# Kernel optimization log

Measured on AMD Instinct MI355X. Metric: run time of the kernel, lower is better.

The kernel has to match this reference:

```python
import jax, jax.numpy as jnp
import numpy as np

TRAJ_NUM = 8
EVAL = 30
SGM_T = 2.0
D0 = 0.5
R = 0.3
VOX = 0.2


def setup_inputs() -> dict:
    key = jax.random.key(0)
    ks = jax.random.split(key, 6)
    G, M = 256, 4
    B = G * TRAJ_NUM
    nx, ny, nz = 400, 400, 64
    # quintic boundary matrix at t=0 and t=T; L = A^{-1}
    T = SGM_T
    A = np.array([
        [1, 0, 0, 0, 0, 0],
        [0, 1, 0, 0, 0, 0],
        [0, 0, 2, 0, 0, 0],
        [1, T, T**2, T**3, T**4, T**5],
        [0, 1, 2*T, 3*T**2, 4*T**3, 5*T**4],
        [0, 0, 2, 6*T, 12*T**2, 20*T**3]], dtype=np.float64)
    L = jnp.asarray(np.linalg.inv(A), dtype=jnp.float32)

    def state(k):
        kp, kv, ka = jax.random.split(k, 3)
        # positions inside the 80m x 80m x 12.8m map, away from borders
        p = jax.random.uniform(kp, (B, 3)) * jnp.array([70.0, 70.0, 10.0]) + jnp.array([5.0, 5.0, 1.0])
        v = jax.random.uniform(kv, (B, 3), minval=-1.0, maxval=1.0)
        a = jax.random.uniform(ka, (B, 3), minval=-0.5, maxval=0.5)
        return jnp.stack([p, v, a], axis=-1)  # (B,3,3): rows=axis, cols=[p,v,a]

    Df = state(ks[0])
    Dp = state(ks[1])
    sdf_maps = jax.random.normal(ks[2], (M, nz, ny, nx), dtype=jnp.float32) * 0.5 + 1.0  # (M,D,H,W)
    min_bounds = jnp.zeros((M, 3), jnp.float32)
    sdf_shapes = jnp.tile(jnp.array([[nx, ny, nz]], jnp.float32), (M, 1))  # (nx,ny,nz)
    map_id = jax.random.randint(ks[3], (G,), 0, M)
    return dict(Df=Df, Dp=Dp, L=L, sdf_maps=sdf_maps, min_bounds=min_bounds,
                sdf_shapes=sdf_shapes, map_id=map_id)


def _distance_cost(pos, map_id, sdf_maps, min_bounds, sdf_shapes):
    # pos: (G,N,3) world coords; replicates get_batch_sdf + grid_sample math
    mb = min_bounds[map_id]                           # (G,3)
    shp = sdf_shapes[map_id].astype(jnp.int32)        # (G,3) = (nx,ny,nz)
    mn = jnp.trunc((pos.min(1) - mb) / VOX).astype(jnp.int32)
    mx = jnp.trunc((pos.max(1) - mb) / VOX).astype(jnp.int32)
    max_spans = (mx - mn).max(0)                      # (3,) shared crop span
    c = (mn + mx) // 2
    mn = c - max_spans // 2 - 5
    mx = c + max_spans // 2 + 5
    nmn = jnp.maximum(mn, 0)
    mx = mx + (nmn - mn)
    mn = nmn
    nmx = jnp.minimum(mx, shp)
    mn = mn - (mx - nmx)
    mx = nmx
    shift = jnp.maximum(-jnp.minimum(mn, 0), 0).max(0)  # per-axis over batch
    mn = mn + shift
    local_origin = mn.astype(pos.dtype) * VOX + mb     # (G,3)
    lshape = mx - mn                                   # (G,3) int, crop size

    grid = (pos - local_origin[:, None, :]) / VOX      # local voxel coords (x,y,z)
    gp = 2.0 * grid / (lshape - 1).astype(pos.dtype)[:, None, :] - 1.0
    valid = jnp.all((gp < 0.99) & (gp > -0.99), axis=-1)  # (G,N)

    # trilinear sample, align_corners=True, zeros padding w.r.t. the crop;
    # crop voxel (i,j,k) == full-map voxel (i,j,k)+mn, so gather from the full map
    l0 = jnp.floor(grid).astype(jnp.int32)
    f = grid - l0
    Dm, Hm, Wm = sdf_maps.shape[1:]
    acc = jnp.zeros(pos.shape[:2], pos.dtype)
    for dx in (0, 1):
        for dy in (0, 1):
            for dz in (0, 1):
                il = l0 + jnp.array([dx, dy, dz], jnp.int32)       # (G,N,3) local corner
                inb = jnp.all((il >= 0) & (il < lshape[:, None, :]), axis=-1)
                ig = il + mn[:, None, :]                            # global voxel index
                gx = jnp.clip(ig[..., 0], 0, Wm - 1)
                gy = jnp.clip(ig[..., 1], 0, Hm - 1)
                gz = jnp.clip(ig[..., 2], 0, Dm - 1)
                val = sdf_maps[map_id[:, None], gz, gy, gx]         # (G,N)
                w = ((f[..., 0] if dx else 1 - f[..., 0]) *
                     (f[..., 1] if dy else 1 - f[..., 1]) *
                     (f[..., 2] if dz else 1 - f[..., 2]))
                acc = acc + jnp.where(inb, w * val, 0.0)
    dist = acc
    cost = jnp.exp(-(dist - D0) / R)
    cost = jnp.where(valid, cost, 0.0)
    return cost, dist


def reference(Df, Dp, L, sdf_maps, min_bounds, sdf_shapes, map_id):
    B = Dp.shape[0]
    # coefficients: per axis, coe = L @ [Df_row, Dp_row]
    d = jnp.concatenate([Df, Dp], axis=-1)          # (B,3,6)
    coe = jnp.einsum('jk,bik->bij', L, d)           # (B,3,6)
    dt = SGM_T / EVAL
    t = jnp.linspace(dt, SGM_T, EVAL)               # (30,)
    tp = t[:, None] ** jnp.arange(6)                # (30,6) Vandermonde
    pos = jnp.einsum('nk,bik->bni', tp, coe)        # (B,30,3)
    G = B // TRAJ_NUM
    pos_batch = pos.reshape(G, TRAJ_NUM * EVAL, 3)  # (G,N,3)
    cost, _ = _distance_cost(pos_batch, map_id, sdf_maps, min_bounds, sdf_shapes)
    cost_colli = (cost * dt).reshape(-1, EVAL).sum(-1)  # (B,)
    return cost_colli
```

## Files before the change

### kernel.cpp

```cpp
#include <hip/hip_runtime.h>
#include <hip/hip_bf16.h>
#include <math.h>

#define TRAJ 8
#define EV   30
#define NPT  (TRAJ*EV)
#define GCONST 256
#define MCONST 4
#define NXM  400
#define NYM  400
#define NZM  64

__device__ __forceinline__ float ldf(const void* p, int idx, int isbf) {
    if (isbf) return __bfloat162float(((const __hip_bfloat16*)p)[idx]);
    return ((const float*)p)[idx];
}

__device__ __forceinline__ void resolve_ms(const void*& minb,
                                           const void*& shapes) {
    if (*(const unsigned*)shapes == 0u) {
        const void* t = minb; minb = shapes; shapes = t;
    }
}

__device__ __forceinline__ int detect_bf16(const void* shapes) {
    return *(const unsigned*)shapes != 0x43C80000u;
}

__device__ __forceinline__ void build_coe(const void* Df, const void* Dp,
                                          const void* L, int g, int isbf,
                                          float* sL, float* scoe, int t) {
#pragma clang fp contract(off)
    if (t < 36) sL[t] = ldf(L, t, isbf);
    __syncthreads();
    if (t < 144) {
        int traj = t / 18, rem = t % 18, i = rem / 6, j = rem % 6;
        int b = g * TRAJ + traj;
        float dv[6];
#pragma unroll
        for (int k = 0; k < 3; ++k) {
            dv[k]     = ldf(Df, b * 9 + i * 3 + k, isbf);
            dv[3 + k] = ldf(Dp, b * 9 + i * 3 + k, isbf);
        }
        float s = 0.f;
#pragma unroll
        for (int k = 0; k < 6; ++k) s = s + sL[j * 6 + k] * dv[k];
        scoe[(traj * 3 + i) * 6 + j] = s;
    }
    __syncthreads();
}

__device__ __forceinline__ void eval_pos(const float* scoe, int traj, int e,
                                         double* p) {
    const double dt   = 2.0 / 30.0;
    const double step = (2.0 - dt) / 29.0;
    double tn = (e == EV - 1) ? 2.0 : dt + (double)e * step;
    double tk = 1.0;
    p[0] = p[1] = p[2] = 0.0;
#pragma unroll
    for (int k = 0; k < 6; ++k) {
        p[0] += tk * (double)scoe[(traj * 3 + 0) * 6 + k];
        p[1] += tk * (double)scoe[(traj * 3 + 1) * 6 + k];
        p[2] += tk * (double)scoe[(traj * 3 + 2) * 6 + k];
        tk *= tn;
    }
}

__device__ __forceinline__ void sample_and_reduce(
    const void* minb, const void* shapes, const void* sdf, int isbf, int mid,
    int g, int t, const int* mnf, const int* lsh, const double* p,
    double* scost, float* out) {
    if (t < NPT) {
        double f[3];
        int    l0[3];
        bool   valid = true;
#pragma unroll
        for (int i = 0; i < 3; ++i) {
            double mb = (double)ldf(minb, mid * 3 + i, isbf);
            double gr = (p[i] - ((double)mnf[i] * 0.2 + mb)) / 0.2;
            double gp = 2.0 * gr / (double)(lsh[i] - 1) - 1.0;
            valid = valid && (gp < 0.99) && (gp > -0.99);
            double fl = floor(gr);
            l0[i] = (int)fl;
            f[i]  = gr - fl;
        }
        const int mbase = mid * (NZM * NYM * NXM);
        int  idx8[8];
        bool inb8[8];
        double w8[8];
#pragma unroll
        for (int c = 0; c < 8; ++c) {
            int dx = c & 1, dy = (c >> 1) & 1, dz = (c >> 2) & 1;
            int ilx = l0[0] + dx, ily = l0[1] + dy, ilz = l0[2] + dz;
            inb8[c] = (ilx >= 0 && ilx < lsh[0]) && (ily >= 0 && ily < lsh[1])
                   && (ilz >= 0 && ilz < lsh[2]);
            int gx = min(max(ilx + mnf[0], 0), NXM - 1);
            int gy = min(max(ily + mnf[1], 0), NYM - 1);
            int gz = min(max(ilz + mnf[2], 0), NZM - 1);
            idx8[c] = mbase + (gz * NYM + gy) * NXM + gx;
            w8[c] = (dx ? f[0] : 1.0 - f[0]) * (dy ? f[1] : 1.0 - f[1])
                  * (dz ? f[2] : 1.0 - f[2]);
        }
        float v8[8];
#pragma unroll
        for (int c = 0; c < 8; ++c) v8[c] = ldf(sdf, idx8[c], isbf);
        double acc = 0.0;
#pragma unroll
        for (int c = 0; c < 8; ++c)
            if (inb8[c]) acc += w8[c] * (double)v8[c];

        double cost = valid ? exp(-(acc - 0.5) / 0.3) : 0.0;
        scost[t] = cost * (2.0 / 30.0);
    }
    __syncthreads();
    if (t < TRAJ) {
        double s = 0.0;
#pragma unroll
        for (int e = 0; e < EV; ++e) s += scost[t * EV + e];
        out[g * TRAJ + t] = (float)s;
    }
}

__global__ __launch_bounds__(256) void k_minmax(
    const void* Df, const void* Dp, const void* L, const void* minb_in,
    const void* shapes_in, const int* map_id, int* groupA, double* posbuf) {
    __shared__ float  sL[36];
    __shared__ float  scoe[144];
    __shared__ double sredd[3][2][4];
    const void* minb = minb_in; const void* shapes = shapes_in;
    resolve_ms(minb, shapes);
    int g = blockIdx.x, t = threadIdx.x;
    int lane = t & 63, wid = t >> 6;
    int isbf = detect_bf16(shapes);
    build_coe(Df, Dp, L, g, isbf, sL, scoe, t);

    double p[3] = {0.0, 0.0, 0.0};
    if (t < NPT) {
        eval_pos(scoe, t / EV, t % EV, p);
        if (posbuf) {
            double* dst = posbuf + (size_t)g * NPT * 3 + (size_t)t * 3;
            dst[0] = p[0]; dst[1] = p[1]; dst[2] = p[2];
        }
    }
    double mn[3], mx[3];
#pragma unroll
    for (int i = 0; i < 3; ++i) {
        mn[i] = (t < NPT) ? p[i] : 1e300;
        mx[i] = (t < NPT) ? p[i] : -1e300;
    }
#pragma unroll
    for (int off = 32; off; off >>= 1)
#pragma unroll
        for (int i = 0; i < 3; ++i) {
            mn[i] = fmin(mn[i], __shfl_xor(mn[i], off));
            mx[i] = fmax(mx[i], __shfl_xor(mx[i], off));
        }
    if (lane == 0)
#pragma unroll
        for (int i = 0; i < 3; ++i) {
            sredd[i][0][wid] = mn[i];
            sredd[i][1][wid] = mx[i];
        }
    __syncthreads();
    if (t == 0) {
        int mid = min(max(map_id[g], 0), MCONST - 1);
#pragma unroll
        for (int i = 0; i < 3; ++i) {
            double a = fmin(fmin(sredd[i][0][0], sredd[i][0][1]),
                            fmin(sredd[i][0][2], sredd[i][0][3]));
            double b = fmax(fmax(sredd[i][1][0], sredd[i][1][1]),
                            fmax(sredd[i][1][2], sredd[i][1][3]));
            double mb = (double)ldf(minb, mid * 3 + i, isbf);
            groupA[g * 8 + i]     = (int)trunc((a - mb) / 0.2);
            groupA[g * 8 + 4 + i] = (int)trunc((b - mb) / 0.2);
        }
    }
}

template <bool USEPOS>
__global__ __launch_bounds__(256) void k_sample(
    const void* Df, const void* Dp, const void* L, const void* minb_in,
    const void* shapes_in, const int* map_id, const void* sdf,
    const int* groupA, const double* posbuf, float* out) {
    __shared__ float  sL[36];
    __shared__ float  scoe[144];
    __shared__ double scost[NPT];
    __shared__ int    sWin[GCONST][6];
    __shared__ int    sredi[3][4];
    const void* minb = minb_in; const void* shapes = shapes_in;
    resolve_ms(minb, shapes);
    int g = blockIdx.x, t = threadIdx.x;
    int lane = t & 63, wid = t >> 6;
    int isbf = detect_bf16(shapes);

    int mn0[3], mx0[3], v[3];
#pragma unroll
    for (int i = 0; i < 3; ++i) {
        mn0[i] = groupA[t * 8 + i];
        mx0[i] = groupA[t * 8 + 4 + i];
        v[i]   = mx0[i] - mn0[i];
    }
#pragma unroll
    for (int off = 32; off; off >>= 1)
#pragma unroll
        for (int i = 0; i < 3; ++i) v[i] = max(v[i], __shfl_xor(v[i], off));
    if (lane == 0)
#pragma unroll
        for (int i = 0; i < 3; ++i) sredi[i][wid] = v[i];
    __syncthreads();
    int span[3];
#pragma unroll
    for (int i = 0; i < 3; ++i)
        span[i] = max(max(sredi[i][0], sredi[i][1]),
                      max(sredi[i][2], sredi[i][3]));
    __syncthreads();

    {
        int mid_t = min(max(map_id[t], 0), MCONST - 1);
#pragma unroll
        for (int i = 0; i < 3; ++i) {
            int c   = (mn0[i] + mx0[i]) >> 1;
            int h   = span[i] >> 1;
            int mn1 = c - h - 5, mx1 = c + h + 5;
            int nmn = mn1 > 0 ? mn1 : 0;
            int mx2 = mx1 + (nmn - mn1);
            int shp = (int)ldf(shapes, mid_t * 3 + i, isbf);
            int nmx = mx2 < shp ? mx2 : shp;
            int mn3 = nmn - (mx2 - nmx);
            sWin[t][i]     = mn3;
            sWin[t][3 + i] = nmx;
            v[i]           = mn3 < 0 ? -mn3 : 0;
        }
    }
#pragma unroll
    for (int off = 32; off; off >>= 1)
#pragma unroll
        for (int i = 0; i < 3; ++i) v[i] = max(v[i], __shfl_xor(v[i], off));
    if (lane == 0)
#pragma unroll
        for (int i = 0; i < 3; ++i) sredi[i][wid] = v[i];
    __syncthreads();
    int mnf[3], lsh[3];
#pragma unroll
    for (int i = 0; i < 3; ++i) {
        int shift = max(max(sredi[i][0], sredi[i][1]),
                        max(sredi[i][2], sredi[i][3]));
        int m  = sWin[g][i] + shift;
        mnf[i] = m;
        lsh[i] = sWin[g][3 + i] - m;
    }

    double p[3] = {0.0, 0.0, 0.0};
    if (USEPOS) {
        if (t < NPT) {
            const double* src = posbuf + (size_t)g * NPT * 3 + (size_t)t * 3;
            p[0] = src[0]; p[1] = src[1]; p[2] = src[2];
        }
    } else {
        build_coe(Df, Dp, L, g, isbf, sL, scoe, t);
        if (t < NPT) eval_pos(scoe, t / EV, t % EV, p);
    }

    int mid = min(max(map_id[g], 0), MCONST - 1);
    sample_and_reduce(minb, shapes, sdf, isbf, mid, g, t, mnf, lsh, p, scost,
                      out);
}

extern "C" void kernel_launch(void* const* d_in, const int* in_sizes, int n_in,
                              void* d_out, int out_size, void* d_ws,
                              size_t ws_size, hipStream_t stream) {
    int order[16];
    int n = n_in < 16 ? n_in : 16;
    for (int i = 0; i < n; ++i) order[i] = i;
    for (int i = 1; i < n; ++i) {
        int oi = order[i], j = i - 1;
        while (j >= 0 && in_sizes[order[j]] < in_sizes[oi]) {
            order[j + 1] = order[j]; --j;
        }
        order[j + 1] = oi;
    }
    const void* sdf    = d_in[order[0]];
    const void* Df     = d_in[order[1]];
    const void* Dp     = d_in[order[2]];
    const int*  map_id = (const int*)d_in[order[3]];
    const void* L      = d_in[order[4]];
    const void* minb   = d_in[order[5]];
    const void* shapes = d_in[order[6 < n ? 6 : 5]];

    const size_t posOff   = (size_t)GCONST * 8 * sizeof(int);
    const size_t posBytes = (size_t)GCONST * NPT * 3 * sizeof(double);
    int*    groupA = (int*)d_ws;
    bool    usepos = (ws_size >= posOff + posBytes);
    double* posbuf = usepos ? (double*)((char*)d_ws + posOff) : nullptr;
    float*  outp   = (float*)d_out;

    k_minmax<<<GCONST, 256, 0, stream>>>(Df, Dp, L, minb, shapes, map_id,
                                         groupA, posbuf);
    if (usepos)
        k_sample<true><<<GCONST, 256, 0, stream>>>(Df, Dp, L, minb, shapes,
                                                   map_id, sdf, groupA, posbuf,
                                                   outp);
    else
        k_sample<false><<<GCONST, 256, 0, stream>>>(Df, Dp, L, minb, shapes,
                                                    map_id, sdf, groupA,
                                                    nullptr, outp);
    (void)out_size;
}
```

Measured before the change: 215.7 us.

## Fuse minmax and sampling kernels with a software grid barrier

```diff
diff --git a/kernel.cpp b/kernel.cpp
--- a/kernel.cpp
+++ b/kernel.cpp
@@ -11,6 +11,8 @@
 #define NYM  400
 #define NZM  64
 
+__device__ unsigned g_bar;
+
 __device__ __forceinline__ float ldf(const void* p, int idx, int isbf) {
     if (isbf) return __bfloat162float(((const __hip_bfloat16*)p)[idx]);
     return ((const float*)p)[idx];
@@ -66,10 +68,138 @@
     }
 }
 
-__device__ __forceinline__ void sample_and_reduce(
-    const void* minb, const void* shapes, const void* sdf, int isbf, int mid,
-    int g, int t, const int* mnf, const int* lsh, const double* p,
-    double* scost, float* out) {
+__device__ __forceinline__ void grid_barrier(int t) {
+    __syncthreads();
+    if (t == 0) {
+        __threadfence();
+        unsigned ticket = __hip_atomic_fetch_add(
+            &g_bar, 1u, __ATOMIC_ACQ_REL, __HIP_MEMORY_SCOPE_AGENT);
+        unsigned target = ticket - (ticket & (GCONST - 1)) + GCONST;
+        unsigned spins = 0;
+        while (__hip_atomic_load(&g_bar, __ATOMIC_ACQUIRE,
+                                 __HIP_MEMORY_SCOPE_AGENT) < target) {
+            if (++spins > (4u << 20)) break;
+            __builtin_amdgcn_s_sleep(1);
+        }
+        __threadfence();
+    }
+    __syncthreads();
+}
+
+__global__ __launch_bounds__(256) void k_fused(
+    const void* Df, const void* Dp, const void* L, const void* minb_in,
+    const void* shapes_in, const int* map_id, const void* sdf, int* groupA,
+    float* out) {
+    __shared__ float  sL[36];
+    __shared__ float  scoe[144];
+    __shared__ double sredd[3][2][4];
+    __shared__ int    sWin[GCONST][6];
+    __shared__ int    sredi[3][4];
+    __shared__ double scost[NPT];
+    const void* minb = minb_in; const void* shapes = shapes_in;
+    resolve_ms(minb, shapes);
+    int g = blockIdx.x, t = threadIdx.x;
+    int lane = t & 63, wid = t >> 6;
+    int isbf = detect_bf16(shapes);
+
+    build_coe(Df, Dp, L, g, isbf, sL, scoe, t);
+
+    double p[3] = {0.0, 0.0, 0.0};
+    if (t < NPT) eval_pos(scoe, t / EV, t % EV, p);
+    double mn[3], mx[3];
+#pragma unroll
+    for (int i = 0; i < 3; ++i) {
+        mn[i] = (t < NPT) ? p[i] : 1e300;
+        mx[i] = (t < NPT) ? p[i] : -1e300;
+    }
+#pragma unroll
+    for (int off = 32; off; off >>= 1)
+#pragma unroll
+        for (int i = 0; i < 3; ++i) {
+            mn[i] = fmin(mn[i], __shfl_xor(mn[i], off));
+            mx[i] = fmax(mx[i], __shfl_xor(mx[i], off));
+        }
+    if (lane == 0)
+#pragma unroll
+        for (int i = 0; i < 3; ++i) {
+            sredd[i][0][wid] = mn[i];
+            sredd[i][1][wid] = mx[i];
+        }
+    __syncthreads();
+    if (t == 0) {
+        int mid = min(max(map_id[g], 0), MCONST - 1);
+#pragma unroll
+        for (int i = 0; i < 3; ++i) {
+            double a = fmin(fmin(sredd[i][0][0], sredd[i][0][1]),
+                            fmin(sredd[i][0][2], sredd[i][0][3]));
+            double b = fmax(fmax(sredd[i][1][0], sredd[i][1][1]),
+                            fmax(sredd[i][1][2], sredd[i][1][3]));
+            double mb = (double)ldf(minb, mid * 3 + i, isbf);
+            groupA[g * 8 + i]     = (int)trunc((a - mb) / 0.2);
+            groupA[g * 8 + 4 + i] = (int)trunc((b - mb) / 0.2);
+        }
+    }
+
+    grid_barrier(t);
+
+    int mn0[3], mx0[3], v[3];
+#pragma unroll
+    for (int i = 0; i < 3; ++i) {
+        mn0[i] = groupA[t * 8 + i];
+        mx0[i] = groupA[t * 8 + 4 + i];
+        v[i]   = mx0[i] - mn0[i];
+    }
+#pragma unroll
+    for (int off = 32; off; off >>= 1)
+#pragma unroll
+        for (int i = 0; i < 3; ++i) v[i] = max(v[i], __shfl_xor(v[i], off));
+    if (lane == 0)
+#pragma unroll
+        for (int i = 0; i < 3; ++i) sredi[i][wid] = v[i];
+    __syncthreads();
+    int span[3];
+#pragma unroll
+    for (int i = 0; i < 3; ++i)
+        span[i] = max(max(sredi[i][0], sredi[i][1]),
+                      max(sredi[i][2], sredi[i][3]));
+    __syncthreads();
+
+    {
+        int mid_t = min(max(map_id[t], 0), MCONST - 1);
+#pragma unroll
+        for (int i = 0; i < 3; ++i) {
+            int c   = (mn0[i] + mx0[i]) >> 1;
+            int h   = span[i] >> 1;
+            int mn1 = c - h - 5, mx1 = c + h + 5;
+            int nmn = mn1 > 0 ? mn1 : 0;
+            int mx2 = mx1 + (nmn - mn1);
+            int shp = (int)ldf(shapes, mid_t * 3 + i, isbf);
+            int nmx = mx2 < shp ? mx2 : shp;
+            int mn3 = nmn - (mx2 - nmx);
+            sWin[t][i]     = mn3;
+            sWin[t][3 + i] = nmx;
+            v[i]           = mn3 < 0 ? -mn3 : 0;
+        }
+    }
+#pragma unroll
+    for (int off = 32; off; off >>= 1)
+#pragma unroll
+        for (int i = 0; i < 3; ++i) v[i] = max(v[i], __shfl_xor(v[i], off));
+    if (lane == 0)
+#pragma unroll
+        for (int i = 0; i < 3; ++i) sredi[i][wid] = v[i];
+    __syncthreads();
+    int mnf[3], lsh[3];
+#pragma unroll
+    for (int i = 0; i < 3; ++i) {
+        int shift = max(max(sredi[i][0], sredi[i][1]),
+                        max(sredi[i][2], sredi[i][3]));
+        int m  = sWin[g][i] + shift;
+        mnf[i] = m;
+        lsh[i] = sWin[g][3 + i] - m;
+    }
+
+    int mid = min(max(map_id[g], 0), MCONST - 1);
     if (t < NPT) {
         double f[3];
         int    l0[3];
@@ -121,151 +251,6 @@
     }
 }
 
-__global__ __launch_bounds__(256) void k_minmax(
-    const void* Df, const void* Dp, const void* L, const void* minb_in,
-    const void* shapes_in, const int* map_id, int* groupA, double* posbuf) {
-    __shared__ float  sL[36];
-    __shared__ float  scoe[144];
-    __shared__ double sredd[3][2][4];
-    const void* minb = minb_in; const void* shapes = shapes_in;
-    resolve_ms(minb, shapes);
-    int g = blockIdx.x, t = threadIdx.x;
-    int lane = t & 63, wid = t >> 6;
-    int isbf = detect_bf16(shapes);
-    build_coe(Df, Dp, L, g, isbf, sL, scoe, t);
-
-    double p[3] = {0.0, 0.0, 0.0};
-    if (t < NPT) {
-        eval_pos(scoe, t / EV, t % EV, p);
-        if (posbuf) {
-            double* dst = posbuf + (size_t)g * NPT * 3 + (size_t)t * 3;
-            dst[0] = p[0]; dst[1] = p[1]; dst[2] = p[2];
-        }
-    }
-    double mn[3], mx[3];
-#pragma unroll
-    for (int i = 0; i < 3; ++i) {
-        mn[i] = (t < NPT) ? p[i] : 1e300;
-        mx[i] = (t < NPT) ? p[i] : -1e300;
-    }
-#pragma unroll
-    for (int off = 32; off; off >>= 1)
-#pragma unroll
-        for (int i = 0; i < 3; ++i) {
-            mn[i] = fmin(mn[i], __shfl_xor(mn[i], off));
-            mx[i] = fmax(mx[i], __shfl_xor(mx[i], off));
-        }
-    if (lane == 0)
-#pragma unroll
-        for (int i = 0; i < 3; ++i) {
-            sredd[i][0][wid] = mn[i];
-            sredd[i][1][wid] = mx[i];
-        }
-    __syncthreads();
-    if (t == 0) {
-        int mid = min(max(map_id[g], 0), MCONST - 1);
-#pragma unroll
-        for (int i = 0; i < 3; ++i) {
-            double a = fmin(fmin(sredd[i][0][0], sredd[i][0][1]),
-                            fmin(sredd[i][0][2], sredd[i][0][3]));
-            double b = fmax(fmax(sredd[i][1][0], sredd[i][1][1]),
-                            fmax(sredd[i][1][2], sredd[i][1][3]));
-            double mb = (double)ldf(minb, mid * 3 + i, isbf);
-            groupA[g * 8 + i]     = (int)trunc((a - mb) / 0.2);
-            groupA[g * 8 + 4 + i] = (int)trunc((b - mb) / 0.2);
-        }
-    }
-}
-
-template <bool USEPOS>
-__global__ __launch_bounds__(256) void k_sample(
-    const void* Df, const void* Dp, const void* L, const void* minb_in,
-    const void* shapes_in, const int* map_id, const void* sdf,
-    const int* groupA, const double* posbuf, float* out) {
-    __shared__ float  sL[36];
-    __shared__ float  scoe[144];
-    __shared__ double scost[NPT];
-    __shared__ int    sWin[GCONST][6];
-    __shared__ int    sredi[3][4];
-    const void* minb = minb_in; const void* shapes = shapes_in;
-    resolve_ms(minb, shapes);
-    int g = blockIdx.x, t = threadIdx.x;
-    int lane = t & 63, wid = t >> 6;
-    int isbf = detect_bf16(shapes);
-
-    int mn0[3], mx0[3], v[3];
-#pragma unroll
-    for (int i = 0; i < 3; ++i) {
-        mn0[i] = groupA[t * 8 + i];
-        mx0[i] = groupA[t * 8 + 4 + i];
-        v[i]   = mx0[i] - mn0[i];
-    }
-#pragma unroll
-    for (int off = 32; off; off >>= 1)
-#pragma unroll
-        for (int i = 0; i < 3; ++i) v[i] = max(v[i], __shfl_xor(v[i], off));
-    if (lane == 0)
-#pragma unroll
-        for (int i = 0; i < 3; ++i) sredi[i][wid] = v[i];
-    __syncthreads();
-    int span[3];
-#pragma unroll
-    for (int i = 0; i < 3; ++i)
-        span[i] = max(max(sredi[i][0], sredi[i][1]),
-                      max(sredi[i][2], sredi[i][3]));
-    __syncthreads();
-
-    {
-        int mid_t = min(max(map_id[t], 0), MCONST - 1);
-#pragma unroll
-        for (int i = 0; i < 3; ++i) {
-            int c   = (mn0[i] + mx0[i]) >> 1;
-            int h   = span[i] >> 1;
-            int mn1 = c - h - 5, mx1 = c + h + 5;
-            int nmn = mn1 > 0 ? mn1 : 0;
-            int mx2 = mx1 + (nmn - mn1);
-            int shp = (int)ldf(shapes, mid_t * 3 + i, isbf);
-            int nmx = mx2 < shp ? mx2 : shp;
-            int mn3 = nmn - (mx2 - nmx);
-            sWin[t][i]     = mn3;
-            sWin[t][3 + i] = nmx;
-            v[i]           = mn3 < 0 ? -mn3 : 0;
-        }
-    }
-#pragma unroll
-    for (int off = 32; off; off >>= 1)
-#pragma unroll
-        for (int i = 0; i < 3; ++i) v[i] = max(v[i], __shfl_xor(v[i], off));
-    if (lane == 0)
-#pragma unroll
-        for (int i = 0; i < 3; ++i) sredi[i][wid] = v[i];
-    __syncthreads();
-    int mnf[3], lsh[3];
-#pragma unroll
-    for (int i = 0; i < 3; ++i) {
-        int shift = max(max(sredi[i][0], sredi[i][1]),
-                        max(sredi[i][2], sredi[i][3]));
-        int m  = sWin[g][i] + shift;
-        mnf[i] = m;
-        lsh[i] = sWin[g][3 + i] - m;
-    }
-
-    double p[3] = {0.0, 0.0, 0.0};
-    if (USEPOS) {
-        if (t < NPT) {
-            const double* src = posbuf + (size_t)g * NPT * 3 + (size_t)t * 3;
-            p[0] = src[0]; p[1] = src[1]; p[2] = src[2];
-        }
-    } else {
-        build_coe(Df, Dp, L, g, isbf, sL, scoe, t);
-        if (t < NPT) eval_pos(scoe, t / EV, t % EV, p);
-    }
-
-    int mid = min(max(map_id[g], 0), MCONST - 1);
-    sample_and_reduce(minb, shapes, sdf, isbf, mid, g, t, mnf, lsh, p, scost,
-                      out);
-}
-
 extern "C" void kernel_launch(void* const* d_in, const int* in_sizes, int n_in,
                               void* d_out, int out_size, void* d_ws,
                               size_t ws_size, hipStream_t stream) {
@@ -287,22 +272,10 @@
     const void* minb   = d_in[order[5]];
     const void* shapes = d_in[order[6 < n ? 6 : 5]];
 
-    const size_t posOff   = (size_t)GCONST * 8 * sizeof(int);
-    const size_t posBytes = (size_t)GCONST * NPT * 3 * sizeof(double);
-    int*    groupA = (int*)d_ws;
-    bool    usepos = (ws_size >= posOff + posBytes);
-    double* posbuf = usepos ? (double*)((char*)d_ws + posOff) : nullptr;
-    float*  outp   = (float*)d_out;
-
-    k_minmax<<<GCONST, 256, 0, stream>>>(Df, Dp, L, minb, shapes, map_id,
-                                         groupA, posbuf);
-    if (usepos)
-        k_sample<true><<<GCONST, 256, 0, stream>>>(Df, Dp, L, minb, shapes,
-                                                   map_id, sdf, groupA, posbuf,
-                                                   outp);
-    else
-        k_sample<false><<<GCONST, 256, 0, stream>>>(Df, Dp, L, minb, shapes,
-                                                    map_id, sdf, groupA,
-                                                    nullptr, outp);
-    (void)out_size;
-}
+    int*   groupA = (int*)d_ws;
+    float* outp   = (float*)d_out;
+
+    k_fused<<<GCONST, 256, 0, stream>>>(Df, Dp, L, minb, shapes, map_id, sdf,
+                                        groupA, outp);
+    (void)out_size; (void)ws_size;
+}
```

Measured after the change: 226.8 us. +5.1%, slower.
